# Kernel optimization log

Measured on AMD Instinct MI355X. Metric: run time of the kernel, lower is better.

The kernel has to match this reference:

```python
import jax, jax.numpy as jnp
import numpy as np

C, NC, B, T, H, W = 64, 4, 4, 8, 96, 96
BT = B * T
_DN = ('NCDHW', 'OIDHW', 'NCDHW')


def setup_inputs() -> dict:
    key = jax.random.key(0)
    ks = jax.random.split(key, 16)
    r = lambda i, shape, s=0.02: jax.random.normal(ks[i], shape, jnp.float32) * s
    f32 = jnp.float32
    return {
        'x': jax.random.normal(ks[0], (BT, C, H, W), f32),
        't': T,
        'temporal_kernels': r(1, (NC, C)),            # (num_components, C) per-channel kernel scale
        'kernel_weights': jnp.ones((NC,), f32),
        'length_scales': jnp.ones((NC,), f32),
        'temporal_basis': r(2, (C, T)),               # (C, 8) learned temporal basis
        'sc_w1': r(3, (C // 8, C), 0.05), 'sc_b1': jnp.zeros((C // 8,), f32),
        'sc_w2': r(4, (2 * C, C // 8), 0.05), 'sc_b2': jnp.zeros((2 * C,), f32),
        'diff_w': r(5, (C, 1, 3, 1, 1), 0.1),         # depthwise temporal conv
        'diff_gamma': jnp.ones((C,), f32), 'diff_beta': jnp.zeros((C,), f32),
        'diff_mean': r(6, (C,), 0.1),
        'diff_var': jnp.ones((C,), f32) + 0.1 * jax.random.uniform(ks[7], (C,), f32),
        'unc_w1': r(8, (C // 4, C), 0.05), 'unc_b1': jnp.zeros((C // 4,), f32),
        'unc_w2': r(9, (2, C // 4), 0.05), 'unc_b2': jnp.zeros((2,), f32),
        'pool_w': r(10, (C, C, 3, 1, 1), 0.02), 'pool_b': jnp.zeros((C,), f32),
        'proj_w': r(11, (C, C), 0.05),                # spectral-normalized 1x1x1 conv
        'bn_gamma': jnp.ones((C,), f32), 'bn_beta': jnp.zeros((C,), f32),
        'bn_mean': r(12, (C,), 0.1),
        'bn_var': jnp.ones((C,), f32) + 0.1 * jax.random.uniform(ks[13], (C,), f32),
        'temperature': jnp.float32(1.0),
    }


def _bc(v):
    return v[None, :, None, None, None]


def reference(x, t, temporal_kernels, kernel_weights, length_scales, temporal_basis,
              sc_w1, sc_b1, sc_w2, sc_b2,
              diff_w, diff_gamma, diff_beta, diff_mean, diff_var,
              unc_w1, unc_b1, unc_w2, unc_b2,
              pool_w, pool_b, proj_w,
              bn_gamma, bn_beta, bn_mean, bn_var, temperature):
    bt, c, h, w = x.shape
    b = bt // t
    x5 = x.reshape(b, t, c, h, w).transpose(0, 2, 1, 3, 4)   # (b,c,t,h,w)

    # --- Gaussian process temporal attention: per-channel (t,t) RBF mixture kernel ---
    ti = jnp.arange(t, dtype=x.dtype)
    dt2 = (ti[:, None] - ti[None, :]) ** 2                    # (t,t)
    ls = jnp.exp(length_scales)                               # (nc,)
    rbf = jnp.exp(-dt2[None] / (2.0 * ls[:, None, None] ** 2))  # (nc,t,t)
    wts = jax.nn.softmax(kernel_weights)
    K = jnp.einsum('i,ic,ist->cst', wts, temporal_kernels, rbf)  # (c,t,t)
    gp = jnp.einsum('cst,bctn->bcsn', K, x5.reshape(b, c, t, h * w)).reshape(b, c, t, h, w)

    # --- stochastic temporal sampling (eval: deterministic importance mask) ---
    mask = jax.nn.softmax(temporal_basis.mean(axis=0))        # (t,)
    stoch = x5 * mask[None, None, :, None, None]

    # --- spatial covariance gate (global pooled MLP -> sigmoid gate) ---
    g = x5.mean(axis=(2, 3, 4))                               # (b,c)
    h1 = jax.nn.gelu(g @ sc_w1.T + sc_b1, approximate=False)
    cov = h1 @ sc_w2.T + sc_b2                                # (b,2c); second half = cov_var
    cov_w = jax.nn.sigmoid(cov[:, c:])[:, :, None, None, None]
    fused0 = gp * cov_w + stoch * (1.0 - cov_w)

    # --- diffusion: depthwise temporal conv + BN(eval) + GELU ---
    d = jax.lax.conv_general_dilated(fused0, diff_w, (1, 1, 1), ((1, 1), (0, 0), (0, 0)),
                                     dimension_numbers=_DN, feature_group_count=c)
    d = _bc(diff_gamma) * (d - _bc(diff_mean)) / jnp.sqrt(_bc(diff_var) + 1e-5) + _bc(diff_beta)
    d = jax.nn.gelu(d, approximate=False)

    # --- uncertainty head + precision-weighted fusion ---
    u = jax.nn.gelu(jnp.einsum('bcthw,oc->bothw', d, unc_w1) + _bc(unc_b1), approximate=False)
    u = jnp.einsum('bcthw,oc->bothw', u, unc_w2) + _bc(unc_b2)  # (b,2,t,h,w)
    mu, var = u[:, :1], u[:, 1:]
    prec = 1.0 / (var + 1e-6)
    fused = (mu * prec + d) / (prec + 1.0)

    # --- temporal pool: temporal conv then global spatial mean ---
    p = jax.lax.conv_general_dilated(fused, pool_w, (1, 1, 1), ((1, 1), (0, 0), (0, 0)),
                                     dimension_numbers=_DN) + _bc(pool_b)
    out = fused + p.mean(axis=(3, 4), keepdims=True)

    # --- spectral-normalized 1x1x1 projection + BN(eval) ---
    sigma = jnp.linalg.svd(proj_w, compute_uv=False)[0]
    out = jnp.einsum('bcthw,oc->bothw', out, proj_w / sigma)
    out = _bc(bn_gamma) * (out - _bc(bn_mean)) / jnp.sqrt(_bc(bn_var) + 1e-5) + _bc(bn_beta)

    out = out.transpose(0, 2, 1, 3, 4).reshape(bt, c, h, w)
    return x + jnp.tanh(temperature) * out
```

## Files before the change

kernel.cpp:

```cpp
#include <hip/hip_runtime.h>
#include <math.h>

#define C64 64
#define NCK 4
#define BB  4
#define TT  8
#define HH  96
#define WW  96
#define HW  9216
#define CHW (C64*HW)
#define NTILE 32
#define NBLK_PER_B (HW/NTILE)

#define OFF_GSUM 0
#define OFF_S    256
#define OFF_COVW 2304
#define OFF_K    2560
#define OFF_MASK 6656
#define OFF_AC   6664
#define OFF_BC   6728
#define OFF_P2   6792
#define OFF_B2   10888
#define OFF_BIAS3 10952
#define OFF_P2BF 13000
#define ZERO_N   2304

typedef __attribute__((ext_vector_type(8))) short short8;
typedef __attribute__((ext_vector_type(4))) float f32x4;

__device__ __forceinline__ float gelu_f(float v) {
    return 0.5f * v * (1.0f + erff(v * 0.70710678118654752f));
}
__device__ __forceinline__ unsigned short f2bf(float f) {
    union { float f; unsigned int u; } v; v.f = f;
    unsigned int r = (v.u + 0x7fffu + ((v.u >> 16) & 1u)) >> 16;
    return (unsigned short)r;
}
__device__ __forceinline__ float bf2f(unsigned short h) {
    union { unsigned int u; float f; } v; v.u = ((unsigned int)h) << 16;
    return v.f;
}
__device__ __forceinline__ int swz(int tn, int c) {
    return (tn << 6) + (c ^ ((tn & 7) << 3));
}

__global__ __launch_bounds__(256) void k1_gsum(const float* __restrict__ x,
                                               float* __restrict__ ws) {
    const int blk = blockIdx.x;
    const float4* p = reinterpret_cast<const float4*>(x + (size_t)blk * HW);
    float s = 0.f;
    for (int i = threadIdx.x; i < HW / 4; i += 256) {
        float4 v = p[i];
        s += v.x + v.y + v.z + v.w;
    }
    #pragma unroll
    for (int off = 32; off; off >>= 1) s += __shfl_down(s, off, 64);
    __shared__ float part[4];
    const int wid = threadIdx.x >> 6, lane = threadIdx.x & 63;
    if (lane == 0) part[wid] = s;
    __syncthreads();
    if (threadIdx.x == 0) {
        float t = part[0] + part[1] + part[2] + part[3];
        int c = blk % C64;
        int b = (blk / C64) / TT;
        atomicAdd(ws + OFF_GSUM + b * C64 + c, t);
    }
}

__global__ __launch_bounds__(256) void k2_prep(
    const float* __restrict__ tk, const float* __restrict__ kw,
    const float* __restrict__ lsc, const float* __restrict__ tb,
    const float* __restrict__ sc_w1, const float* __restrict__ sc_b1,
    const float* __restrict__ sc_w2, const float* __restrict__ sc_b2,
    const float* __restrict__ diff_gamma, const float* __restrict__ diff_beta,
    const float* __restrict__ diff_mean, const float* __restrict__ diff_var,
    const float* __restrict__ proj_w,
    const float* __restrict__ bn_gamma, const float* __restrict__ bn_beta,
    const float* __restrict__ bn_mean, const float* __restrict__ bn_var,
    const float* __restrict__ temperature,
    float* __restrict__ ws) {
    __shared__ float gsh[BB * C64];
    __shared__ float h1[BB][8];
    __shared__ float wtss[NCK], lss[NCK];
    __shared__ float Msh[64 * 64];
    __shared__ float M2sh[64 * 64];
    __shared__ float v0[64], v1[64];
    __shared__ float lamsh;
    const int tid = threadIdx.x;

    gsh[tid] = ws[OFF_GSUM + tid] * (1.0f / ((float)TT * (float)HW));
    __syncthreads();

    if (tid < BB * 8) {
        int b = tid >> 3, j = tid & 7;
        float a = sc_b1[j];
        for (int c = 0; c < C64; c++) a += gsh[b * C64 + c] * sc_w1[j * C64 + c];
        h1[b][j] = gelu_f(a);
    }
    if (tid == 0) {
        float mx = -1e30f;
        for (int i = 0; i < NCK; i++) mx = fmaxf(mx, kw[i]);
        float e[NCK], s = 0.f;
        for (int i = 0; i < NCK; i++) { e[i] = expf(kw[i] - mx); s += e[i]; }
        for (int i = 0; i < NCK; i++) { wtss[i] = e[i] / s; lss[i] = expf(lsc[i]); }
    }
    if (tid == 1) {
        float m[TT], mx = -1e30f;
        for (int t = 0; t < TT; t++) {
            float a = 0.f;
            for (int c = 0; c < C64; c++) a += tb[c * TT + t];
            m[t] = a * (1.0f / (float)C64);
            mx = fmaxf(mx, m[t]);
        }
        float s = 0.f;
        for (int t = 0; t < TT; t++) { m[t] = expf(m[t] - mx); s += m[t]; }
        for (int t = 0; t < TT; t++) ws[OFF_MASK + t] = m[t] / s;
    }
    __syncthreads();

    {
        int b = tid >> 6, c = tid & 63;
        float a = sc_b2[C64 + c];
        for (int j = 0; j < 8; j++) a += h1[b][j] * sc_w2[(C64 + c) * 8 + j];
        ws[OFF_COVW + b * C64 + c] = 1.f / (1.f + expf(-a));
    }
    for (int q = tid; q < C64 * TT * TT; q += 256) {
        int c = q >> 6, s8 = (q >> 3) & 7, t8 = q & 7;
        float dt = (float)(s8 - t8);
        float dt2 = dt * dt;
        float a = 0.f;
        for (int i = 0; i < NCK; i++)
            a += wtss[i] * tk[i * C64 + c] * expf(-dt2 / (2.f * lss[i] * lss[i]));
        ws[OFF_K + q] = a;
    }
    if (tid < C64) {
        float ac = diff_gamma[tid] * rsqrtf(diff_var[tid] + 1e-5f);
        ws[OFF_AC + tid] = ac;
        ws[OFF_BC + tid] = diff_beta[tid] - ac * diff_mean[tid];
    }
    for (int q = tid; q < 4096; q += 256) {
        int i = q >> 6, j = q & 63;
        float a = 0.f;
        for (int k = 0; k < 64; k++) a += proj_w[k * 64 + i] * proj_w[k * 64 + j];
        Msh[q] = a;
    }
    __syncthreads();
    for (int q = tid; q < 4096; q += 256) {
        int i = q >> 6, j = q & 63;
        float a = 0.f;
        for (int k = 0; k < 64; k++) a += Msh[i * 64 + k] * Msh[k * 64 + j];
        M2sh[q] = a;
    }
    if (tid < 64) v0[tid] = 1.f;
    __syncthreads();
    for (int it = 0; it < 24; ++it) {
        float y = 0.f;
        if (tid < 64) {
            for (int k = 0; k < 64; k++) y += M2sh[k * 64 + tid] * v0[k];
        }
        float yy = y * y;
        #pragma unroll
        for (int off = 32; off; off >>= 1) yy += __shfl_down(yy, off, 64);
        float nrm = __shfl(yy, 0, 64);
        if (tid < 64) v1[tid] = y * rsqrtf(fmaxf(nrm, 1e-30f));
        __syncthreads();
        if (tid < 64) v0[tid] = v1[tid];
        __syncthreads();
    }
    {
        float a = 0.f;
        if (tid < 64) {
            for (int k = 0; k < 64; k++) a += Msh[k * 64 + tid] * v0[k];
            a *= v0[tid];
        }
        #pragma unroll
        for (int off = 32; off; off >>= 1) a += __shfl_down(a, off, 64);
        if (tid == 0) lamsh = a;
    }
    __syncthreads();
    const float sigma = sqrtf(fmaxf(lamsh, 1e-30f));
    const float tau = tanhf(temperature[0]);
    if (tid < 64) {
        float gp = bn_gamma[tid] * rsqrtf(bn_var[tid] + 1e-5f);
        ws[OFF_B2 + tid] = tau * (bn_beta[tid] - gp * bn_mean[tid]);
    }
    {
        short* p2b = (short*)(ws + OFF_P2BF);
        for (int q = tid; q < 4096; q += 256) {
            int o = q >> 6;
            float gp = bn_gamma[o] * rsqrtf(bn_var[o] + 1e-5f);
            float v = tau * gp * proj_w[q] / sigma;
            ws[OFF_P2 + q] = v;
            p2b[q] = (short)f2bf(v);
        }
    }
}

__global__ __launch_bounds__(256) void k3_main(
    const float* __restrict__ x, const float* __restrict__ diff_w,
    const float* __restrict__ unc_w1, const float* __restrict__ unc_b1,
    const float* __restrict__ unc_w2, const float* __restrict__ unc_b2,
    const float* __restrict__ ws, float* __restrict__ out) {
    __shared__ short dls[256 * 64];
    const int tile = blockIdx.x;
    const int b = tile / NBLK_PER_B;
    const int n0 = (tile % NBLK_PER_B) * NTILE;
    const int tid = threadIdx.x;
    const int nloc = tid & 31;

    {
        const int n = n0 + nloc;
        float mk[TT];
        #pragma unroll
        for (int t = 0; t < TT; t++) mk[t] = ws[OFF_MASK + t];
        #pragma unroll
        for (int p = 0; p < 8; p++) {
            const int c = (tid >> 5) + (p << 3);
            float xr[TT];
            #pragma unroll
            for (int t = 0; t < TT; t++)
                xr[t] = x[(size_t)((b * TT + t) * C64 + c) * HW + n];
            const float cw = ws[OFF_COVW + b * C64 + c];
            const float* kr = ws + OFF_K + c * (TT * TT);
            float f0[TT];
            #pragma unroll
            for (int s = 0; s < TT; s++) {
                float a = 0.f;
                #pragma unroll
                for (int t = 0; t < TT; t++) a += kr[s * TT + t] * xr[t];
                f0[s] = a * cw + xr[s] * mk[s] * (1.f - cw);
            }
            const float w0 = diff_w[c * 3 + 0], w1 = diff_w[c * 3 + 1], w2 = diff_w[c * 3 + 2];
            const float ac = ws[OFF_AC + c], bc = ws[OFF_BC + c];
            #pragma unroll
            for (int t = 0; t < TT; t++) {
                float pre = w1 * f0[t];
                if (t > 0)      pre += w0 * f0[t - 1];
                if (t < TT - 1) pre += w2 * f0[t + 1];
                dls[swz(t * 32 + nloc, c)] = (short)f2bf(gelu_f(ac * pre + bc));
            }
        }
    }
    __syncthreads();

    {
        const int t = tid >> 5;
        float dcol[C64];
        #pragma unroll
        for (int j = 0; j < 8; j++) {
            short8 v = *(const short8*)(dls + swz(tid, j * 8));
            #pragma unroll
            for (int i = 0; i < 8; i++) dcol[j * 8 + i] = bf2f((unsigned short)v[i]);
        }
        float u1[16];
        #pragma unroll
        for (int o = 0; o < 16; o++) {
            float a = unc_b1[o];
            const float* wr = unc_w1 + o * C64;
            #pragma unroll
            for (int c = 0; c < C64; c++) a += wr[c] * dcol[c];
            u1[o] = gelu_f(a);
        }
        float mu = unc_b2[0], va = unc_b2[1];
        #pragma unroll
        for (int o = 0; o < 16; o++) {
            mu += unc_w2[o] * u1[o];
            va += unc_w2[16 + o] * u1[o];
        }
        const float vp = va + 1e-6f;
        const float inv = 1.f / (1.f + vp);
        const float alpha = vp * inv;
        const float beta = mu * inv;

        #pragma unroll
        for (int j = 0; j < 8; j++) {
            short8 wv;
            #pragma unroll
            for (int i = 0; i < 8; i++) {
                float f = alpha * dcol[j * 8 + i] + beta;
                wv[i] = (short)f2bf(f);
                float v = f;
                v += __shfl_xor(v, 1);
                v += __shfl_xor(v, 2);
                v += __shfl_xor(v, 4);
                v += __shfl_xor(v, 8);
                v += __shfl_xor(v, 16);
                if ((tid & 31) == 0)
                    atomicAdd((float*)ws + OFF_S + (b * C64 + (j * 8 + i)) * TT + t, v);
            }
            *(short8*)(dls + swz(tid, j * 8)) = wv;
        }
    }
    __syncthreads();

    {
        const int w = tid >> 6;
        const int l = tid & 63;
        const int l15 = l & 15;
        const int lg = (l >> 4) & 3;
        const short* P2B = (const short*)(ws + OFF_P2BF);
        f32x4 acc[4][4] = {};
        #pragma unroll
        for (int kh = 0; kh < 2; ++kh) {
            const int cb = kh * 32 + lg * 8;
            short8 bfr[4];
            #pragma unroll
            for (int nt = 0; nt < 4; ++nt) {
                const int tn = w * 64 + nt * 16 + l15;
                bfr[nt] = *(const short8*)(dls + swz(tn, cb));
            }
            #pragma unroll
            for (int mt = 0; mt < 4; ++mt) {
                const int o = mt * 16 + l15;
                short8 afr = *(const short8*)(P2B + o * 64 + cb);
                #pragma unroll
                for (int nt = 0; nt < 4; ++nt)
                    acc[mt][nt] = __builtin_amdgcn_mfma_f32_16x16x32_bf16(
                        afr, bfr[nt], acc[mt][nt], 0, 0, 0);
            }
        }
        #pragma unroll
        for (int nt = 0; nt < 4; ++nt) {
            const int t = 2 * w + (nt >> 1);
            const int nl = (nt & 1) * 16 + l15;
            #pragma unroll
            for (int mt = 0; mt < 4; ++mt) {
                #pragma unroll
                for (int j = 0; j < 4; ++j) {
                    const int o = mt * 16 + lg * 4 + j;
                    const size_t idx = (size_t)((b * TT + t) * C64 + o) * HW + n0 + nl;
                    out[idx] = x[idx] + acc[mt][nt][j];
                }
            }
        }
    }
}

__global__ __launch_bounds__(64) void k4_bias(
    const float* __restrict__ pool_w, const float* __restrict__ pool_b,
    float* __restrict__ ws) {
    const int b = blockIdx.x >> 3, t = blockIdx.x & 7;
    const int o = threadIdx.x;
    __shared__ float pm[C64];
    float a = 0.f;
    for (int k = 0; k < 3; k++) {
        int tt = t + k - 1;
        if (tt < 0 || tt >= TT) continue;
        const float* Sp = ws + OFF_S + b * C64 * TT + tt;
        for (int cp = 0; cp < C64; cp++)
            a += pool_w[(o * C64 + cp) * 3 + k] * Sp[cp * TT];
    }
    pm[o] = pool_b[o] + a * (1.0f / (float)HW);
    __syncthreads();
    float bb = ws[OFF_B2 + o];
    const float* pr = ws + OFF_P2 + o * C64;
    for (int c = 0; c < C64; c++) bb += pr[c] * pm[c];
    ws[OFF_BIAS3 + (b * C64 + o) * TT + t] = bb;
}

__global__ __launch_bounds__(256) void k5_bias(
    const float* __restrict__ ws, float* __restrict__ out) {
    const int plane = blockIdx.x;
    const int o = plane & 63;
    const int bt = plane >> 6;
    const int b = bt >> 3, t = bt & 7;
    const float bias = ws[OFF_BIAS3 + (b * C64 + o) * TT + t];
    float4* p = reinterpret_cast<float4*>(out + (size_t)plane * HW);
    #pragma unroll
    for (int i = 0; i < 9; i++) {
        const int idx = threadIdx.x + i * 256;
        float4 v = p[idx];
        v.x += bias; v.y += bias; v.z += bias; v.w += bias;
        p[idx] = v;
    }
}

extern "C" void kernel_launch(void* const* d_in, const int* in_sizes, int n_in,
                              void* d_out, int out_size, void* d_ws, size_t ws_size,
                              hipStream_t stream) {
    const float* x           = (const float*)d_in[0];
    const float* tk          = (const float*)d_in[2];
    const float* kw          = (const float*)d_in[3];
    const float* lsc         = (const float*)d_in[4];
    const float* tb          = (const float*)d_in[5];
    const float* sc_w1       = (const float*)d_in[6];
    const float* sc_b1       = (const float*)d_in[7];
    const float* sc_w2       = (const float*)d_in[8];
    const float* sc_b2       = (const float*)d_in[9];
    const float* diff_w      = (const float*)d_in[10];
    const float* diff_gamma  = (const float*)d_in[11];
    const float* diff_beta   = (const float*)d_in[12];
    const float* diff_mean   = (const float*)d_in[13];
    const float* diff_var    = (const float*)d_in[14];
    const float* unc_w1      = (const float*)d_in[15];
    const float* unc_b1      = (const float*)d_in[16];
    const float* unc_w2      = (const float*)d_in[17];
    const float* unc_b2      = (const float*)d_in[18];
    const float* pool_w      = (const float*)d_in[19];
    const float* pool_b      = (const float*)d_in[20];
    const float* proj_w      = (const float*)d_in[21];
    const float* bn_gamma    = (const float*)d_in[22];
    const float* bn_beta     = (const float*)d_in[23];
    const float* bn_mean     = (const float*)d_in[24];
    const float* bn_var      = (const float*)d_in[25];
    const float* temperature = (const float*)d_in[26];
    float* ws = (float*)d_ws;
    float* out = (float*)d_out;

    hipMemsetAsync(ws, 0, ZERO_N * sizeof(float), stream);
    k1_gsum<<<dim3(BB * TT * C64), dim3(256), 0, stream>>>(x, ws);
    k2_prep<<<dim3(1), dim3(256), 0, stream>>>(tk, kw, lsc, tb, sc_w1, sc_b1,
                                               sc_w2, sc_b2, diff_gamma, diff_beta,
                                               diff_mean, diff_var, proj_w, bn_gamma,
                                               bn_beta, bn_mean, bn_var, temperature, ws);
    k3_main<<<dim3(BB * NBLK_PER_B), dim3(256), 0, stream>>>(x, diff_w, unc_w1, unc_b1,
                                                             unc_w2, unc_b2, ws, out);
    k4_bias<<<dim3(BB * TT), dim3(64), 0, stream>>>(pool_w, pool_b, ws);
    k5_bias<<<dim3(BB * TT * C64), dim3(256), 0, stream>>>(ws, out);
}
```

Before: 507.8 us.

## Vectorize k3 phase-1 loads, transpose weight tables, cut register pressure

k3_main's first phase now gives each thread one channel and four contiguous pixels. It loads x as float4 and reads the temporal kernel from a channel-minor transposed table in the workspace. The uncertainty head accumulates u1 directly instead of holding a 64-float column, and launch bounds request 4 blocks per CU. k2_prep stages proj_w in shared memory and writes transposed pool_w and proj tables so k4_bias reads coalesced. The aim is wider, coalesced global loads and higher occupancy, at the cost of more workspace and some bank-conflict risk from the strided dls writes.

```diff
diff --git a/kernel.cpp b/kernel.cpp
--- a/kernel.cpp
+++ b/kernel.cpp
@@ -23,6 +23,8 @@
 #define OFF_B2   10888
 #define OFF_BIAS3 10952
 #define OFF_P2BF 13000
+#define OFF_P2T  15048
+#define OFF_POOLT 19144
 #define ZERO_N   2304
 
 typedef __attribute__((ext_vector_type(8))) short short8;
@@ -74,7 +76,7 @@
     const float* __restrict__ sc_w2, const float* __restrict__ sc_b2,
     const float* __restrict__ diff_gamma, const float* __restrict__ diff_beta,
     const float* __restrict__ diff_mean, const float* __restrict__ diff_var,
-    const float* __restrict__ proj_w,
+    const float* __restrict__ proj_w, const float* __restrict__ pool_w,
     const float* __restrict__ bn_gamma, const float* __restrict__ bn_beta,
     const float* __restrict__ bn_mean, const float* __restrict__ bn_var,
     const float* __restrict__ temperature,
@@ -82,6 +84,7 @@
     __shared__ float gsh[BB * C64];
     __shared__ float h1[BB][8];
     __shared__ float wtss[NCK], lss[NCK];
+    __shared__ float Pls[64 * 64];
     __shared__ float Msh[64 * 64];
     __shared__ float M2sh[64 * 64];
     __shared__ float v0[64], v1[64];
@@ -89,6 +92,7 @@
     const int tid = threadIdx.x;
 
     gsh[tid] = ws[OFF_GSUM + tid] * (1.0f / ((float)TT * (float)HW));
+    for (int q = tid; q < 4096; q += 256) Pls[q] = proj_w[q];
     __syncthreads();
 
     if (tid < BB * 8) {
@@ -131,17 +135,21 @@
         float a = 0.f;
         for (int i = 0; i < NCK; i++)
             a += wtss[i] * tk[i * C64 + c] * expf(-dt2 / (2.f * lss[i] * lss[i]));
-        ws[OFF_K + q] = a;
+        ws[OFF_K + (q & 63) * C64 + c] = a;
     }
     if (tid < C64) {
         float ac = diff_gamma[tid] * rsqrtf(diff_var[tid] + 1e-5f);
         ws[OFF_AC + tid] = ac;
         ws[OFF_BC + tid] = diff_beta[tid] - ac * diff_mean[tid];
     }
+    for (int q = tid; q < C64 * C64 * 3; q += 256) {
+        int o = q / 192, r = q % 192, cp = r / 3, k = r % 3;
+        ws[OFF_POOLT + (k * C64 + cp) * C64 + o] = pool_w[q];
+    }
     for (int q = tid; q < 4096; q += 256) {
         int i = q >> 6, j = q & 63;
         float a = 0.f;
-        for (int k = 0; k < 64; k++) a += proj_w[k * 64 + i] * proj_w[k * 64 + j];
+        for (int k = 0; k < 64; k++) a += Pls[k * 64 + i] * Pls[k * 64 + j];
         Msh[q] = a;
     }
     __syncthreads();
@@ -187,16 +195,17 @@
     {
         short* p2b = (short*)(ws + OFF_P2BF);
         for (int q = tid; q < 4096; q += 256) {
-            int o = q >> 6;
+            int o = q >> 6, c = q & 63;
             float gp = bn_gamma[o] * rsqrtf(bn_var[o] + 1e-5f);
-            float v = tau * gp * proj_w[q] / sigma;
+            float v = tau * gp * Pls[q] / sigma;
             ws[OFF_P2 + q] = v;
+            ws[OFF_P2T + c * C64 + o] = v;
             p2b[q] = (short)f2bf(v);
         }
     }
 }
 
-__global__ __launch_bounds__(256) void k3_main(
+__global__ __launch_bounds__(256, 4) void k3_main(
     const float* __restrict__ x, const float* __restrict__ diff_w,
     const float* __restrict__ unc_w1, const float* __restrict__ unc_b1,
     const float* __restrict__ unc_w2, const float* __restrict__ unc_b2,
@@ -206,38 +215,49 @@
     const int b = tile / NBLK_PER_B;
     const int n0 = (tile % NBLK_PER_B) * NTILE;
     const int tid = threadIdx.x;
-    const int nloc = tid & 31;
-
-    {
-        const int n = n0 + nloc;
+
+    {
+        const int cc = tid >> 2;
+        const int nq = tid & 3;
+        const float cw = ws[OFF_COVW + b * C64 + cc];
+        const float ac = ws[OFF_AC + cc], bc = ws[OFF_BC + cc];
+        const float w0 = diff_w[cc * 3 + 0], w1 = diff_w[cc * 3 + 1], w2 = diff_w[cc * 3 + 2];
         float mk[TT];
         #pragma unroll
         for (int t = 0; t < TT; t++) mk[t] = ws[OFF_MASK + t];
         #pragma unroll
-        for (int p = 0; p < 8; p++) {
-            const int c = (tid >> 5) + (p << 3);
-            float xr[TT];
+        for (int q = 0; q < 2; ++q) {
+            const int nb = q * 16 + nq * 4;
+            float4 xr[TT];
             #pragma unroll
             for (int t = 0; t < TT; t++)
-                xr[t] = x[(size_t)((b * TT + t) * C64 + c) * HW + n];
-            const float cw = ws[OFF_COVW + b * C64 + c];
-            const float* kr = ws + OFF_K + c * (TT * TT);
-            float f0[TT];
+                xr[t] = *reinterpret_cast<const float4*>(
+                    x + (size_t)((b * TT + t) * C64 + cc) * HW + n0 + nb);
+            float f0[TT][4];
             #pragma unroll
             for (int s = 0; s < TT; s++) {
-                float a = 0.f;
+                float a0 = 0.f, a1 = 0.f, a2 = 0.f, a3 = 0.f;
                 #pragma unroll
-                for (int t = 0; t < TT; t++) a += kr[s * TT + t] * xr[t];
-                f0[s] = a * cw + xr[s] * mk[s] * (1.f - cw);
-            }
-            const float w0 = diff_w[c * 3 + 0], w1 = diff_w[c * 3 + 1], w2 = diff_w[c * 3 + 2];
-            const float ac = ws[OFF_AC + c], bc = ws[OFF_BC + c];
+                for (int t = 0; t < TT; t++) {
+                    const float kv = ws[OFF_K + (s * TT + t) * C64 + cc];
+                    a0 += kv * xr[t].x; a1 += kv * xr[t].y;
+                    a2 += kv * xr[t].z; a3 += kv * xr[t].w;
+                }
+                const float sm = mk[s] * (1.f - cw);
+                f0[s][0] = a0 * cw + xr[s].x * sm;
+                f0[s][1] = a1 * cw + xr[s].y * sm;
+                f0[s][2] = a2 * cw + xr[s].z * sm;
+                f0[s][3] = a3 * cw + xr[s].w * sm;
+            }
             #pragma unroll
             for (int t = 0; t < TT; t++) {
-                float pre = w1 * f0[t];
-                if (t > 0)      pre += w0 * f0[t - 1];
-                if (t < TT - 1) pre += w2 * f0[t + 1];
-                dls[swz(t * 32 + nloc, c)] = (short)f2bf(gelu_f(ac * pre + bc));
+                #pragma unroll
+                for (int i = 0; i < 4; i++) {
+                    float pre = w1 * f0[t][i];
+                    if (t > 0)      pre += w0 * f0[t - 1][i];
+                    if (t < TT - 1) pre += w2 * f0[t + 1][i];
+                    dls[swz(t * 32 + nb + i, cc)] = (short)f2bf(gelu_f(ac * pre + bc));
+                }
             }
         }
     }
@@ -245,22 +265,22 @@
 
     {
         const int t = tid >> 5;
-        float dcol[C64];
+        float u1[16];
+        #pragma unroll
+        for (int o = 0; o < 16; o++) u1[o] = unc_b1[o];
         #pragma unroll
         for (int j = 0; j < 8; j++) {
             short8 v = *(const short8*)(dls + swz(tid, j * 8));
             #pragma unroll
-            for (int i = 0; i < 8; i++) dcol[j * 8 + i] = bf2f((unsigned short)v[i]);
-        }
-        float u1[16];
-        #pragma unroll
-        for (int o = 0; o < 16; o++) {
-            float a = unc_b1[o];
-            const float* wr = unc_w1 + o * C64;
-            #pragma unroll
-            for (int c = 0; c < C64; c++) a += wr[c] * dcol[c];
-            u1[o] = gelu_f(a);
-        }
+            for (int i = 0; i < 8; i++) {
+                const float dv = bf2f((unsigned short)v[i]);
+                #pragma unroll
+                for (int o = 0; o < 16; o++)
+                    u1[o] += unc_w1[o * C64 + j * 8 + i] * dv;
+            }
+        }
+        #pragma unroll
+        for (int o = 0; o < 16; o++) u1[o] = gelu_f(u1[o]);
         float mu = unc_b2[0], va = unc_b2[1];
         #pragma unroll
         for (int o = 0; o < 16; o++) {
@@ -274,19 +294,20 @@
 
         #pragma unroll
         for (int j = 0; j < 8; j++) {
+            short8 v = *(const short8*)(dls + swz(tid, j * 8));
             short8 wv;
             #pragma unroll
             for (int i = 0; i < 8; i++) {
-                float f = alpha * dcol[j * 8 + i] + beta;
+                const float f = alpha * bf2f((unsigned short)v[i]) + beta;
                 wv[i] = (short)f2bf(f);
-                float v = f;
-                v += __shfl_xor(v, 1);
-                v += __shfl_xor(v, 2);
-                v += __shfl_xor(v, 4);
-                v += __shfl_xor(v, 8);
-                v += __shfl_xor(v, 16);
+                float s = f;
+                s += __shfl_xor(s, 1);
+                s += __shfl_xor(s, 2);
+                s += __shfl_xor(s, 4);
+                s += __shfl_xor(s, 8);
+                s += __shfl_xor(s, 16);
                 if ((tid & 31) == 0)
-                    atomicAdd((float*)ws + OFF_S + (b * C64 + (j * 8 + i)) * TT + t, v);
+                    atomicAdd((float*)ws + OFF_S + (b * C64 + (j * 8 + i)) * TT + t, s);
             }
             *(short8*)(dls + swz(tid, j * 8)) = wv;
         }
@@ -337,8 +358,7 @@
 }
 
 __global__ __launch_bounds__(64) void k4_bias(
-    const float* __restrict__ pool_w, const float* __restrict__ pool_b,
-    float* __restrict__ ws) {
+    const float* __restrict__ pool_b, float* __restrict__ ws) {
     const int b = blockIdx.x >> 3, t = blockIdx.x & 7;
     const int o = threadIdx.x;
     __shared__ float pm[C64];
@@ -346,15 +366,15 @@
     for (int k = 0; k < 3; k++) {
         int tt = t + k - 1;
         if (tt < 0 || tt >= TT) continue;
+        const float* Pk = ws + OFF_POOLT + k * C64 * C64;
         const float* Sp = ws + OFF_S + b * C64 * TT + tt;
         for (int cp = 0; cp < C64; cp++)
-            a += pool_w[(o * C64 + cp) * 3 + k] * Sp[cp * TT];
+            a += Pk[cp * C64 + o] * Sp[cp * TT];
     }
     pm[o] = pool_b[o] + a * (1.0f / (float)HW);
     __syncthreads();
     float bb = ws[OFF_B2 + o];
-    const float* pr = ws + OFF_P2 + o * C64;
-    for (int c = 0; c < C64; c++) bb += pr[c] * pm[c];
+    for (int c = 0; c < C64; c++) bb += ws[OFF_P2T + c * C64 + o] * pm[c];
     ws[OFF_BIAS3 + (b * C64 + o) * TT + t] = bb;
 }
 
@@ -411,10 +431,11 @@
     k1_gsum<<<dim3(BB * TT * C64), dim3(256), 0, stream>>>(x, ws);
     k2_prep<<<dim3(1), dim3(256), 0, stream>>>(tk, kw, lsc, tb, sc_w1, sc_b1,
                                                sc_w2, sc_b2, diff_gamma, diff_beta,
-                                               diff_mean, diff_var, proj_w, bn_gamma,
-                                               bn_beta, bn_mean, bn_var, temperature, ws);
+                                               diff_mean, diff_var, proj_w, pool_w,
+                                               bn_gamma, bn_beta, bn_mean, bn_var,
+                                               temperature, ws);
     k3_main<<<dim3(BB * NBLK_PER_B), dim3(256), 0, stream>>>(x, diff_w, unc_w1, unc_b1,
                                                              unc_w2, unc_b2, ws, out);
-    k4_bias<<<dim3(BB * TT), dim3(64), 0, stream>>>(pool_w, pool_b, ws);
+    k4_bias<<<dim3(BB * TT), dim3(64), 0, stream>>>(pool_b, ws);
     k5_bias<<<dim3(BB * TT * C64), dim3(256), 0, stream>>>(ws, out);
 }
```

After: 562.5 us. 1.11x slower.
